# Kernel tuning notes

Measured on AMD Instinct MI355X. Metric: run time of the kernel, lower is better.

## Reference

```python
import jax, jax.numpy as jnp
from jax import lax
import numpy as np

B, L, D, H, SH = 4, 1024, 512, 8, 256
MLP_H = 4 * D
GAMMA, BETA = 0.1, 1.0
SIG_A, SIG_B = 1.0, 0.5
BIG = 1e9


def setup_inputs() -> dict:
    key = jax.random.key(0)
    ks = jax.random.split(key, 8)

    def lin(k, fin, fout):
        return jax.random.normal(k, (fin, fout), jnp.float32) * (1.0 / np.sqrt(fin))

    inp = {}
    inp["x"] = jax.random.normal(ks[0], (B, L, D), jnp.float32)
    inp["ln1_g"] = jnp.ones((D,), jnp.float32)
    inp["ln1_b"] = jnp.zeros((D,), jnp.float32)
    inp["ln2_g"] = jnp.ones((D,), jnp.float32)
    inp["ln2_b"] = jnp.zeros((D,), jnp.float32)
    inp["qkv_w"] = lin(ks[1], D, 3 * D)
    inp["qkv_b"] = jnp.zeros((3 * D,), jnp.float32)
    inp["proj_w"] = lin(ks[2], D, D)
    inp["proj_b"] = jnp.zeros((D,), jnp.float32)
    inp["fc1_w"] = lin(ks[3], D, MLP_H)
    inp["fc1_b"] = jnp.zeros((MLP_H,), jnp.float32)
    inp["fc2_w"] = lin(ks[4], MLP_H, D)
    inp["fc2_b"] = jnp.zeros((D,), jnp.float32)
    # 4 SigmaNets (norm1, attn, norm2, mlp) stacked on leading axis
    inp["sig_w1"] = jax.random.normal(ks[5], (4, D, SH), jnp.float32) * (1.0 / np.sqrt(D))
    inp["sig_b1"] = jnp.zeros((4, SH), jnp.float32)
    inp["sig_w2"] = jax.random.normal(ks[6], (4, SH, D), jnp.float32) * (1.0 / np.sqrt(SH))
    inp["sig_b2"] = jnp.zeros((4, D), jnp.float32)
    return inp


def layernorm(x, g, b, eps=1e-5):
    m = x.mean(-1, keepdims=True)
    v = ((x - m) ** 2).mean(-1, keepdims=True)
    return (x - m) / jnp.sqrt(v + eps) * g + b


def sigmanet(x, w1, b1, w2, b2):
    # (B,L,D) -> (B,L,1), sigma = a*sigmoid(mean(fc2(relu(fc1(x))))) + b
    h = jax.nn.relu(x @ w1 + b1)
    o = h @ w2 + b2
    m = o.mean(-1, keepdims=True)
    return SIG_A * jax.nn.sigmoid(m) + SIG_B


def attention(x, qkv_w, qkv_b, proj_w, proj_b):
    b_, l_, d_ = x.shape
    hd = d_ // H
    qkv = (x @ qkv_w + qkv_b).reshape(b_, l_, 3, H, hd)
    q, k, v = qkv[:, :, 0], qkv[:, :, 1], qkv[:, :, 2]  # (B,L,H,hd)
    scores = jnp.einsum("bqhd,bkhd->bhqk", q, k) * (hd ** -0.5)
    attn = jax.nn.softmax(scores, axis=-1)
    out = jnp.einsum("bhqk,bkhd->bqhd", attn, v).reshape(b_, l_, d_)
    return out @ proj_w + proj_b


def mlp(x, fc1_w, fc1_b, fc2_w, fc2_b):
    return jax.nn.gelu(x @ fc1_w + fc1_b, approximate=False) @ fc2_w + fc2_b


def soft_dtw(C, gamma):
    # soft-min DP over (B, N, N) cost matrix via anti-diagonal scan
    b_, n_, m_ = C.shape
    i_arr = jnp.arange(n_)

    def step(carry, k):
        d2, d1 = carry  # diagonals k-2, k-1; entry i holds R[i, (k-?)-i]
        j = k - i_arr
        valid = (j >= 0) & (j < m_)
        jc = jnp.clip(j, 0, m_ - 1)
        Cd = jnp.where(valid[None, :], C[:, i_arr, jc], BIG)
        pad = jnp.full((b_, 1), BIG, C.dtype)
        a = jnp.concatenate([pad, d2[:, :-1]], axis=1)  # R[i-1, j-1]
        a = a.at[:, 0].set(jnp.where(k == 0, 0.0, a[:, 0]))  # virtual R[-1,-1]=0
        bdiag = jnp.concatenate([pad, d1[:, :-1]], axis=1)  # R[i-1, j]
        c = d1  # R[i, j-1]
        smin = -gamma * jax.nn.logsumexp(-jnp.stack([a, bdiag, c], 0) / gamma, axis=0)
        new = jnp.where(valid[None, :], Cd + smin, BIG)
        return (d1, new), None

    init = (jnp.full((b_, n_), BIG, C.dtype), jnp.full((b_, n_), BIG, C.dtype))
    (_, last), _ = lax.scan(step, init, jnp.arange(n_ + m_ - 1))
    return last[:, n_ - 1]  # R[N-1, M-1]


def udtw(x, y, sx, sy):
    # pairwise squared distances without (B,L,L,D) intermediate
    x2 = jnp.sum(x * x, -1)  # (B,L)
    y2 = jnp.sum(y * y, -1)
    Dm = x2[:, :, None] + y2[:, None, :] - 2.0 * jnp.einsum("bnd,bmd->bnm", x, y)
    Dm = jnp.maximum(Dm, 0.0)
    Sig = sx ** 2 + jnp.swapaxes(sy, 1, 2) ** 2  # (B,L,L) sigma_i^2 + sigma_j^2
    d = soft_dtw(Dm / Sig, GAMMA)               # uncertainty-weighted distance path
    s = soft_dtw(BETA * jnp.log(Sig), GAMMA)    # sigma regularization path
    return d, s


def reference(x, ln1_g, ln1_b, ln2_g, ln2_b, qkv_w, qkv_b, proj_w, proj_b,
              fc1_w, fc1_b, fc2_w, fc2_b, sig_w1, sig_b1, sig_w2, sig_b2):
    orig = x
    attn_out = attention(layernorm(x, ln1_g, ln1_b), qkv_w, qkv_b, proj_w, proj_b)
    sigma_x = sigmanet(orig, sig_w1[0], sig_b1[0], sig_w2[0], sig_b2[0])
    sigma_attn = sigmanet(attn_out, sig_w1[1], sig_b1[1], sig_w2[1], sig_b2[1])
    d_a, s_a = udtw(orig, attn_out, sigma_x, sigma_attn)
    x = x + attn_out * sigma_attn  # merge_mode == 'mul'
    mlp_out = mlp(layernorm(x, ln2_g, ln2_b), fc1_w, fc1_b, fc2_w, fc2_b)
    sigma_x2 = sigmanet(orig, sig_w1[2], sig_b1[2], sig_w2[2], sig_b2[2])
    sigma_mlp = sigmanet(mlp_out, sig_w1[3], sig_b1[3], sig_w2[3], sig_b2[3])
    d_m, s_m = udtw(orig, mlp_out, sigma_x2, sigma_mlp)
    l_ = x.shape[1]
    aux_loss = (d_a.mean() + s_a.mean() + d_m.mean() + s_m.mean()) / (l_ * l_)
    x = x + mlp_out * sigma_mlp
    return x, aux_loss
```

## Files before the change

kernel.cpp:

```cpp
#include <hip/hip_runtime.h>
#include <math.h>

typedef unsigned short ushort;
typedef __attribute__((ext_vector_type(8))) short short8;
typedef __attribute__((ext_vector_type(4))) short short4v;
typedef __attribute__((ext_vector_type(4))) float f32x4;

#define DEVI static __device__ __forceinline__

constexpr int Bq = 4, Lq = 1024, Dq = 512, Hq = 8, SHq = 256;
constexpr int Mrows = Bq * Lq;
constexpr float BIGF = 1e9f;
constexpr int PSTR = 1048576 + 16;

DEVI float bf2f(ushort u) { union { unsigned u; float f; } v; v.u = ((unsigned)u) << 16; return v.f; }
DEVI float bf2f(short s) { return bf2f((ushort)s); }
DEVI ushort f2bf(float f) {
  union { float f; unsigned u; } v; v.f = f;
  unsigned r = v.u + 0x7fffu + ((v.u >> 16) & 1u);
  return (ushort)(r >> 16);
}
DEVI float wave_sum(float x) { for (int o = 1; o < 64; o <<= 1) x += __shfl_xor(x, o, 64); return x; }
DEVI float readin(const void* p, long i, int isf32) {
  return isf32 ? ((const float*)p)[i] : bf2f(((const ushort*)p)[i]);
}

__global__ void detect_kern(const unsigned* __restrict__ g, int* __restrict__ flag) {
  if (threadIdx.x == 0) flag[0] = (g[0] == 0x3F800000u) ? 1 : 0;
}

struct PrepArgs {
  const void *ln1_g, *ln1_b, *ln2_g, *ln2_b, *qkv_b, *proj_b, *fc1_b, *fc2_b, *sig_b1;
  ushort* csmall;
  const void* x_raw; ushort* x_bf;
  const void *qkv_w, *proj_w, *fc1_w, *fc2_w, *sig_w1;
  ushort *wt_qkv, *wt_proj, *wt_fc1, *wt_fc2, *wt_sig1;
  const void *sig_w2;
  const void *sig_b2;
  float *w2bar, *b2bar;
  const int* flag;
};

DEVI void do_transpose(const void* src, ushort* dst, int R, int C, int bx, int by, int bz, int f,
                       ushort (*t)[65]) {
  const int tx = threadIdx.x & 63, tg = threadIdx.x >> 6;
  const long base = (long)bz * R * C;
  const int r0 = by * 64, c0 = bx * 64;
#pragma unroll
  for (int i = 0; i < 16; ++i) {
    int y = tg * 16 + i;
    float v = readin(src, base + (long)(r0 + y) * C + c0 + tx, f);
    t[y][tx] = f2bf(v);
  }
  __syncthreads();
#pragma unroll
  for (int i = 0; i < 16; ++i) {
    int y = tg * 16 + i;
    dst[base + (long)(c0 + y) * R + r0 + tx] = t[tx][y];
  }
}

__global__ __launch_bounds__(256) void prep_kern(PrepArgs a) {
  __shared__ ushort t[64][65];
  const int bid = blockIdx.x, tid = threadIdx.x;
  const int f = *a.flag;
  if (bid < 9) {
    const int off[10] = {0, 512, 1024, 1536, 2048, 3584, 4096, 6144, 6656, 7680};
    const void* ps[9] = {a.ln1_g, a.ln1_b, a.ln2_g, a.ln2_b, a.qkv_b, a.proj_b, a.fc1_b, a.fc2_b, a.sig_b1};
    const void* s = ps[bid];
    const int n = off[bid + 1] - off[bid];
    for (int i = tid; i < n; i += 256)
      a.csmall[off[bid] + i] = f ? f2bf(((const float*)s)[i]) : ((const ushort*)s)[i];
  } else if (bid < 2057) {
    const long c0 = (long)(bid - 9) * 1024;
    for (int i = tid; i < 1024; i += 256)
      a.x_bf[c0 + i] = f ? f2bf(((const float*)a.x_raw)[c0 + i]) : ((const ushort*)a.x_raw)[c0 + i];
  } else if (bid < 2313) {
    const int wid = tid >> 6, lane = tid & 63;
    const int p = (bid - 2057) * 4 + wid;
    const int k = p & 255, s = p >> 8;
    float acc = 0.f;
#pragma unroll
    for (int i = 0; i < 8; ++i) acc += readin(a.sig_w2, ((long)s * SHq + k) * Dq + lane * 8 + i, f);
    acc = wave_sum(acc);
    if (lane == 0) a.w2bar[s * SHq + k] = acc * (1.f / Dq);
  } else if (bid < 2314) {
    const int wid = tid >> 6, lane = tid & 63;
    float acc = 0.f;
#pragma unroll
    for (int i = 0; i < 8; ++i) acc += readin(a.sig_b2, (long)wid * Dq + lane * 8 + i, f);
    acc = wave_sum(acc);
    if (lane == 0) a.b2bar[wid] = acc * (1.f / Dq);
  } else if (bid < 2506) {
    const int lb = bid - 2314;
    do_transpose(a.qkv_w, a.wt_qkv, 512, 1536, lb % 24, lb / 24, 0, f, t);
  } else if (bid < 2570) {
    const int lb = bid - 2506;
    do_transpose(a.proj_w, a.wt_proj, 512, 512, lb % 8, lb / 8, 0, f, t);
  } else if (bid < 2826) {
    const int lb = bid - 2570;
    do_transpose(a.fc1_w, a.wt_fc1, 512, 2048, lb % 32, lb / 32, 0, f, t);
  } else if (bid < 3082) {
    const int lb = bid - 2826;
    do_transpose(a.fc2_w, a.wt_fc2, 2048, 512, lb % 8, lb / 8, 0, f, t);
  } else {
    const int lb = bid - 3082;
    const int z = lb / 32, rem = lb % 32;
    do_transpose(a.sig_w1, a.wt_sig1, 512, 256, rem % 4, rem / 4, z, f, t);
  }
}

__global__ __launch_bounds__(256) void ln_kern(const ushort* __restrict__ x, const ushort* __restrict__ g,
                                               const ushort* __restrict__ b, ushort* __restrict__ out,
                                               float* __restrict__ x2out) {
  const int row = blockIdx.x * 4 + (threadIdx.x >> 6);
  const int lane = threadIdx.x & 63;
  short8 v = *(const short8*)(x + (long)row * Dq + lane * 8);
  float f[8]; float s = 0.f, s2 = 0.f;
#pragma unroll
  for (int i = 0; i < 8; ++i) { f[i] = bf2f(v[i]); s += f[i]; s2 += f[i] * f[i]; }
  s = wave_sum(s); s2 = wave_sum(s2);
  if (lane == 0) x2out[row] = s2;
  float mean = s * (1.f / Dq);
  float var = s2 * (1.f / Dq) - mean * mean;
  float rstd = rsqrtf(var + 1e-5f);
  short8 gv = *(const short8*)(g + lane * 8);
  short8 bv = *(const short8*)(b + lane * 8);
  short8 o;
#pragma unroll
  for (int i = 0; i < 8; ++i) o[i] = (short)f2bf((f[i] - mean) * rstd * bf2f(gv[i]) + bf2f(bv[i]));
  *(short8*)(out + (long)row * Dq + lane * 8) = o;
}

template<int EPI>
__global__ __launch_bounds__(256) void gemm_kern(
    const ushort* __restrict__ A, int lda, long sA,
    const ushort* __restrict__ Bt, int ldb, long sB,
    const ushort* __restrict__ bias,
    void* __restrict__ Cout, int ldc, long sC, int K,
    const float* __restrict__ vx2, const float* __restrict__ vy2,
    const float* __restrict__ vsx, const float* __restrict__ vsy) {
  constexpr int LDT = 40;
  __shared__ alignas(16) short As[128 * LDT];
  __shared__ alignas(16) short Bs[128 * LDT];
  const int tid = threadIdx.x, lane = tid & 63, wid = tid >> 6;
  const int wr = wid >> 1, wc = wid & 1;
  const int m0 = blockIdx.y * 128, n0 = blockIdx.x * 128;
  const int bz = blockIdx.z;
  const ushort* Ab = A + (long)bz * sA;
  const ushort* Bb = Bt + (long)bz * sB;
  const int sr = tid >> 2, sc = (tid & 3) * 8;
  const int lr = lane & 15, lk = (lane >> 4) * 8;
  f32x4 acc[4][4];
#pragma unroll
  for (int i = 0; i < 4; ++i)
#pragma unroll
    for (int j = 0; j < 4; ++j) acc[i][j] = f32x4{0.f, 0.f, 0.f, 0.f};

  for (int k0 = 0; k0 < K; k0 += 32) {
    short8 a0 = *(const short8*)(Ab + (long)(m0 + sr) * lda + k0 + sc);
    short8 a1 = *(const short8*)(Ab + (long)(m0 + sr + 64) * lda + k0 + sc);
    short8 b0 = *(const short8*)(Bb + (long)(n0 + sr) * ldb + k0 + sc);
    short8 b1 = *(const short8*)(Bb + (long)(n0 + sr + 64) * ldb + k0 + sc);
    __syncthreads();
    *(short8*)&As[sr * LDT + sc] = a0;
    *(short8*)&As[(sr + 64) * LDT + sc] = a1;
    *(short8*)&Bs[sr * LDT + sc] = b0;
    *(short8*)&Bs[(sr + 64) * LDT + sc] = b1;
    __syncthreads();
    short8 af[4], bg[4];
#pragma unroll
    for (int m = 0; m < 4; ++m) af[m] = *(const short8*)&As[(wr * 64 + m * 16 + lr) * LDT + lk];
#pragma unroll
    for (int n = 0; n < 4; ++n) bg[n] = *(const short8*)&Bs[(wc * 64 + n * 16 + lr) * LDT + lk];
#pragma unroll
    for (int m = 0; m < 4; ++m)
#pragma unroll
      for (int n = 0; n < 4; ++n)
        acc[m][n] = __builtin_amdgcn_mfma_f32_16x16x32_bf16(af[m], bg[n], acc[m][n], 0, 0, 0);
  }
  const int lq = (lane >> 4) * 4;
#pragma unroll
  for (int n = 0; n < 4; ++n) {
    const int col = n0 + wc * 64 + n * 16 + lr;
    float bia = 0.f, y2v = 0.f, syv = 0.f;
    if (EPI <= 2) { if (bias) bia = bf2f(bias[col]); }
    if (EPI == 3) { y2v = vy2[(long)bz * Lq + col]; float t = vsy[(long)bz * Lq + col]; syv = t * t; }
#pragma unroll
    for (int m = 0; m < 4; ++m) {
      f32x4 v = acc[m][n];
      if (EPI <= 2) {
#pragma unroll
        for (int q = 0; q < 4; ++q) {
          const int row = m0 + wr * 64 + m * 16 + lq + q;
          float c = v[q] + bia;
          if (EPI == 1) c = fmaxf(c, 0.f);
          if (EPI == 2) c = 0.5f * c * (1.f + erff(c * 0.70710678118654752f));
          ((ushort*)Cout)[(long)bz * sC + (long)row * ldc + col] = f2bf(c);
        }
      } else {
        const int row0 = m0 + wr * 64 + m * 16 + lq;
        f32x4 o;
#pragma unroll
        for (int q = 0; q < 4; ++q) {
          float x2v = vx2[(long)bz * Lq + row0 + q];
          float sxv = vsx[(long)bz * Lq + row0 + q];
          float dm = fmaxf(x2v + y2v - 2.f * v[q], 0.f);
          o[q] = dm / (sxv * sxv + syv);
        }
        *(f32x4*)((float*)Cout + (long)bz * sC + (long)col * 1024 + row0) = o;
      }
    }
  }
}

__global__ __launch_bounds__(256) void attn_kern(const ushort* __restrict__ qkv, ushort* __restrict__ octx) {
  const int qt = blockIdx.x, h = blockIdx.y, b = blockIdx.z;
  const int tid = threadIdx.x, lane = tid & 63, wid = tid >> 6;
  const int lr = lane & 15, lkg = lane >> 4;
  __shared__ alignas(16) short Ks[64 * 72];
  __shared__ alignas(16) short Vt[64 * 72];
  __shared__ alignas(16) short Ps[64 * 72];
  const long qrow0 = (long)b * Lq + qt * 64;
  short8 qf[2];
  {
    const ushort* qp = qkv + (qrow0 + wid * 16 + lr) * 1536 + h * 64;
    qf[0] = *(const short8*)(qp + lkg * 8);
    qf[1] = *(const short8*)(qp + 32 + lkg * 8);
  }
  f32x4 accO[4];
#pragma unroll
  for (int n = 0; n < 4; ++n) accO[n] = f32x4{0.f, 0.f, 0.f, 0.f};
  float mrun[4], lrun[4];
#pragma unroll
  for (int q = 0; q < 4; ++q) { mrun[q] = -1e30f; lrun[q] = 0.f; }

  for (int t = 0; t < 16; ++t) {
    __syncthreads();
#pragma unroll
    for (int i = 0; i < 2; ++i) {
      const int row = (tid >> 3) + i * 32;
      const int c8 = (tid & 7) * 8;
      const long gr = ((long)b * Lq + t * 64 + row) * 1536 + h * 64;
      short8 kv = *(const short8*)(qkv + gr + 512 + c8);
      *(short8*)&Ks[row * 72 + c8] = kv;
      short8 vv = *(const short8*)(qkv + gr + 1024 + c8);
#pragma unroll
      for (int j = 0; j < 8; ++j) Vt[(c8 + j) * 72 + row] = vv[j];
    }
    __syncthreads();
    f32x4 sf[4];
#pragma unroll
    for (int n = 0; n < 4; ++n) {
      sf[n] = f32x4{0.f, 0.f, 0.f, 0.f};
#pragma unroll
      for (int ks = 0; ks < 2; ++ks) {
        short8 bk = *(const short8*)&Ks[(n * 16 + lr) * 72 + ks * 32 + lkg * 8];
        sf[n] = __builtin_amdgcn_mfma_f32_16x16x32_bf16(qf[ks], bk, sf[n], 0, 0, 0);
      }
    }
#pragma unroll
    for (int n = 0; n < 4; ++n)
#pragma unroll
      for (int q = 0; q < 4; ++q) sf[n][q] *= 0.125f;
    float scl[4];
#pragma unroll
    for (int q = 0; q < 4; ++q) {
      float mx = fmaxf(fmaxf(sf[0][q], sf[1][q]), fmaxf(sf[2][q], sf[3][q]));
#pragma unroll
      for (int o = 1; o < 16; o <<= 1) mx = fmaxf(mx, __shfl_xor(mx, o, 64));
      float mnew = fmaxf(mrun[q], mx);
      scl[q] = __expf(mrun[q] - mnew);
      mrun[q] = mnew;
      float rs = 0.f;
#pragma unroll
      for (int n = 0; n < 4; ++n) { float pp = __expf(sf[n][q] - mnew); sf[n][q] = pp; rs += pp; }
#pragma unroll
      for (int o = 1; o < 16; o <<= 1) rs += __shfl_xor(rs, o, 64);
      lrun[q] = lrun[q] * scl[q] + rs;
    }
#pragma unroll
    for (int n = 0; n < 4; ++n)
#pragma unroll
      for (int q = 0; q < 4; ++q) accO[n][q] *= scl[q];
#pragma unroll
    for (int n = 0; n < 4; ++n)
#pragma unroll
      for (int q = 0; q < 4; ++q)
        Ps[(wid * 16 + lkg * 4 + q) * 72 + n * 16 + lr] = (short)f2bf(sf[n][q]);
    short8 pa[2];
    pa[0] = *(const short8*)&Ps[(wid * 16 + lr) * 72 + lkg * 8];
    pa[1] = *(const short8*)&Ps[(wid * 16 + lr) * 72 + 32 + lkg * 8];
#pragma unroll
    for (int n = 0; n < 4; ++n)
#pragma unroll
      for (int ks = 0; ks < 2; ++ks) {
        short8 bv = *(const short8*)&Vt[(n * 16 + lr) * 72 + ks * 32 + lkg * 8];
        accO[n] = __builtin_amdgcn_mfma_f32_16x16x32_bf16(pa[ks], bv, accO[n], 0, 0, 0);
      }
  }
#pragma unroll
  for (int n = 0; n < 4; ++n) {
    const int col = h * 64 + n * 16 + lr;
#pragma unroll
    for (int q = 0; q < 4; ++q) {
      const long row = qrow0 + wid * 16 + lkg * 4 + q;
      octx[row * 512 + col] = f2bf(accO[n][q] / fmaxf(lrun[q], 1e-30f));
    }
  }
}

__global__ __launch_bounds__(256) void rownorm2_kern(const ushort* __restrict__ x, float* __restrict__ out) {
  const int row = blockIdx.x * 4 + (threadIdx.x >> 6), lane = threadIdx.x & 63;
  short8 v = *(const short8*)(x + (long)row * Dq + lane * 8);
  float s = 0.f;
#pragma unroll
  for (int i = 0; i < 8; ++i) { float f = bf2f(v[i]); s += f * f; }
  s = wave_sum(s);
  if (lane == 0) out[row] = s;
}

__global__ __launch_bounds__(256) void sigma_reduce_kern(const ushort* __restrict__ h, const float* __restrict__ w2bar,
                                                         const float* __restrict__ b2bar, int set,
                                                         float* __restrict__ sigma) {
  const int row = blockIdx.x * 4 + (threadIdx.x >> 6), lane = threadIdx.x & 63;
  short4v hv = *(const short4v*)(h + (long)row * SHq + lane * 4);
  float s = 0.f;
#pragma unroll
  for (int i = 0; i < 4; ++i) s += bf2f(hv[i]) * w2bar[lane * 4 + i];
  s = wave_sum(s);
  if (lane == 0) {
    float m = s + b2bar[set];
    sigma[(long)set * Mrows + row] = 1.f / (1.f + __expf(-m)) + 0.5f;
  }
}

__global__ __launch_bounds__(256) void fuse1_kern(const ushort* __restrict__ x, const ushort* __restrict__ attn,
                                                  const float* __restrict__ sig, const ushort* __restrict__ g,
                                                  const ushort* __restrict__ bb, void* __restrict__ x1out,
                                                  ushort* __restrict__ xn2, const int* __restrict__ flag) {
  const int row = blockIdx.x * 4 + (threadIdx.x >> 6), lane = threadIdx.x & 63;
  const int isf32 = *flag;
  const float sg = sig[row];
  short8 xv = *(const short8*)(x + (long)row * Dq + lane * 8);
  short8 av = *(const short8*)(attn + (long)row * Dq + lane * 8);
  float f[8]; float s = 0.f, s2 = 0.f;
#pragma unroll
  for (int i = 0; i < 8; ++i) {
    f[i] = bf2f(xv[i]) + bf2f(av[i]) * sg;
    s += f[i]; s2 += f[i] * f[i];
  }
  if (isf32) {
    float* o32 = (float*)x1out + (long)row * Dq + lane * 8;
    *(f32x4*)o32 = f32x4{f[0], f[1], f[2], f[3]};
    *(f32x4*)(o32 + 4) = f32x4{f[4], f[5], f[6], f[7]};
  } else {
    short8 xo;
#pragma unroll
    for (int i = 0; i < 8; ++i) xo[i] = (short)f2bf(f[i]);
    *(short8*)((ushort*)x1out + (long)row * Dq + lane * 8) = xo;
  }
  s = wave_sum(s); s2 = wave_sum(s2);
  float mean = s * (1.f / Dq);
  float var = s2 * (1.f / Dq) - mean * mean;
  float rstd = rsqrtf(var + 1e-5f);
  short8 gv = *(const short8*)(g + lane * 8);
  short8 bv = *(const short8*)(bb + lane * 8);
  short8 o;
#pragma unroll
  for (int i = 0; i < 8; ++i) o[i] = (short)f2bf((f[i] - mean) * rstd * bf2f(gv[i]) + bf2f(bv[i]));
  *(short8*)(xn2 + (long)row * Dq + lane * 8) = o;
}

__global__ __launch_bounds__(256) void fuse2_kern(const ushort* __restrict__ mlp,
                                                  const float* __restrict__ sig, void* __restrict__ out,
                                                  const int* __restrict__ flag) {
  const int row = blockIdx.x * 4 + (threadIdx.x >> 6), lane = threadIdx.x & 63;
  const int isf32 = *flag;
  const float sg = sig[row];
  short8 mv = *(const short8*)(mlp + (long)row * Dq + lane * 8);
  if (isf32) {
    float* o32 = (float*)out + (long)row * Dq + lane * 8;
    f32x4 a = *(const f32x4*)o32;
    f32x4 b = *(const f32x4*)(o32 + 4);
#pragma unroll
    for (int i = 0; i < 4; ++i) a[i] += bf2f(mv[i]) * sg;
#pragma unroll
    for (int i = 0; i < 4; ++i) b[i] += bf2f(mv[4 + i]) * sg;
    *(f32x4*)o32 = a;
    *(f32x4*)(o32 + 4) = b;
  } else {
    ushort* o16 = (ushort*)out + (long)row * Dq + lane * 8;
    short8 xv = *(const short8*)o16;
    short8 o;
#pragma unroll
    for (int i = 0; i < 8; ++i) o[i] = (short)f2bf(bf2f(xv[i]) + bf2f(mv[i]) * sg);
    *(short8*)o16 = o;
  }
}

__global__ __launch_bounds__(128, 1) void dtw_kern(const float* __restrict__ Cta, const float* __restrict__ Ctm,
                                                   const float* __restrict__ sigma, float* __restrict__ res) {
  const int sid = blockIdx.x >> 2, b = blockIdx.x & 3;
  const int tid = threadIdx.x, lane = tid & 63, wid = tid >> 6;
  const bool isS = (sid & 1);
  __shared__ alignas(16) float smemf[18432];
  constexpr float LN2 = 0.69314718055994531f;

  float cur[16];
#pragma unroll
  for (int r = 0; r < 16; ++r) cur[r] = BIGF;
  float A = BIGF;
  float B = BIGF;
  float D = (lane == 0) ? 0.f : BIGF;

  if (!isS) {
    const float* Ct = ((sid == 0) ? Cta : Ctm) + (long)b * PSTR;

#define PRODUCE2(S0)                                                           \
    {                                                                          \
      f32x4 L[4][8];                                                           \
      _Pragma("unroll")                                                        \
      for (int j = 0; j < 4; ++j) {                                            \
        const int ss = (S0) + j;                                               \
        int cA = 2 * ss - 2 * lane;                                            \
        int cB = cA + 1;                                                       \
        cA = cA < 0 ? 0 : (cA > 1023 ? 1023 : cA);                             \
        cB = cB < 0 ? 0 : (cB > 1023 ? 1023 : cB);                             \
        const float* gA = Ct + (long)cA * 1024 + lane * 16;                    \
        const float* gB = Ct + (long)cB * 1024 + lane * 16;                    \
        _Pragma("unroll")                                                      \
        for (int q = 0; q < 4; ++q) { L[j][q] = *(const f32x4*)(gA + q * 4);   \
                                      L[j][4 + q] = *(const f32x4*)(gB + q * 4); } \
      }                                                                        \
      __builtin_amdgcn_sched_barrier(0);                                       \
      _Pragma("unroll")                                                        \
      for (int j = 0; j < 4; ++j) {                                            \
        float* lp = &smemf[(((S0) + j) & 7) * 2304 + lane * 36];               \
        _Pragma("unroll")                                                      \
        for (int q = 0; q < 4; ++q) { *(f32x4*)(lp + q * 4) = L[j][q];         \
                                      *(f32x4*)(lp + 16 + q * 4) = L[j][4 + q]; } \
      }                                                                        \
    }

#define LOADR(RA, RB, S)                                                       \
    {                                                                          \
      const float* lp = &smemf[((S) & 7) * 2304 + lane * 36];                  \
      _Pragma("unroll")                                                        \
      for (int q = 0; q < 4; ++q) { RA[q] = *(const f32x4*)(lp + q * 4);       \
                                    RB[q] = *(const f32x4*)(lp + 16 + q * 4); } \
    }

#define DCHAIN2(S, RA, RB, CHK)                                                \
    {                                                                          \
      const int c1 = 2 * (S) - 2 * lane;                                       \
      const bool v1 = (unsigned)c1 < 1024u;                                    \
      const bool v2 = (unsigned)(c1 + 1) < 1024u;                              \
      float above = A, diag = D;                                               \
      _Pragma("unroll")                                                        \
      for (int i = 0; i < 16; ++i) {                                           \
        float tmp = cur[i];                                                    \
        float v = RA[i >> 2][i & 3] + fminf(fminf(above, tmp), diag);          \
        cur[i] = (CHK) ? (v1 ? v : tmp) : v;                                   \
        diag = tmp; above = v;                                                 \
      }                                                                        \
      float bot1 = cur[15];                                                    \
      above = B; diag = A;                                                     \
      _Pragma("unroll")                                                        \
      for (int i = 0; i < 16; ++i) {                                           \
        float tmp = cur[i];                                                    \
        float v = RB[i >> 2][i & 3] + fminf(fminf(above, tmp), diag);          \
        cur[i] = (CHK) ? (v2 ? v : tmp) : v;                                   \
        diag = tmp; above = v;                                                 \
      }                                                                        \
      float bot2 = cur[15];                                                    \
      D = B;                                                                   \
      float sA = __shfl_up(bot1, 1, 64);                                       \
      float sB = __shfl_up(bot2, 1, 64);                                       \
      A = (lane == 0) ? BIGF : sA;                                             \
      B = (lane == 0) ? BIGF : sB;                                             \
    }

#define DPHASE4(S0, CHK)                                                       \
    {                                                                          \
      f32x4 pa[4], pb[4], qa[4], qb[4];                                        \
      LOADR(pa, pb, (S0) + 0)                                                  \
      LOADR(qa, qb, (S0) + 1)                                                  \
      DCHAIN2((S0) + 0, pa, pb, CHK)                                           \
      LOADR(pa, pb, (S0) + 2)                                                  \
      DCHAIN2((S0) + 1, qa, qb, CHK)                                           \
      LOADR(qa, qb, (S0) + 3)                                                  \
      DCHAIN2((S0) + 2, pa, pb, CHK)                                           \
      DCHAIN2((S0) + 3, qa, qb, CHK)                                           \
    }

    if (wid == 1) PRODUCE2(0)
    __syncthreads();
#pragma clang loop unroll(disable)
    for (int p = 0; p < 16; ++p) {
      if (wid == 1) { PRODUCE2(4 * p + 4) } else { DPHASE4(4 * p, 1) }
      __syncthreads();
    }
#pragma clang loop unroll(disable)
    for (int p = 16; p < 128; ++p) {
      if (wid == 1) { PRODUCE2(4 * p + 4) } else { DPHASE4(4 * p, 0) }
      __syncthreads();
    }
#pragma clang loop unroll(disable)
    for (int p = 128; p < 144; ++p) {
      if (wid == 1) { if (p < 143) PRODUCE2(4 * p + 4) } else { DPHASE4(4 * p, 1) }
      __syncthreads();
    }
#undef PRODUCE2
#undef LOADR
#undef DCHAIN2
#undef DPHASE4
    if (wid == 0 && lane == 63) res[blockIdx.x] = cur[15];
  } else {
    const int sxset = (sid == 1) ? 0 : 2;
    const float* sxv = sigma + (long)sxset * Mrows + b * Lq;
    const float* syv = sigma + (long)(sxset + 1) * Mrows + b * Lq;
    for (int i = tid; i < Lq; i += 128) { float v = syv[i]; smemf[i] = v * v; }
    __syncthreads();
    if (wid == 1) return;
    float sx2[16];
#pragma unroll
    for (int r = 0; r < 16; ++r) { float t = sxv[16 * lane + r]; sx2[r] = t * t; }
    int ia = -2 * lane; ia = ia < 0 ? 0 : ia;
    int ib = 1 - 2 * lane; ib = ib < 0 ? 0 : ib;
    float syA = smemf[ia], syB = smemf[ib];

#define SSTEP2(S, CHK)                                                         \
    {                                                                          \
      int na = 2 * ((S) + 1) - 2 * lane; na = na < 0 ? 0 : (na > 1023 ? 1023 : na); \
      int nb = na + 1; nb = nb > 1023 ? 1023 : nb;                             \
      float syA_n = smemf[na], syB_n = smemf[nb];                              \
      const int c1 = 2 * (S) - 2 * lane;                                       \
      const bool v1 = (unsigned)c1 < 1024u;                                    \
      const bool v2 = (unsigned)(c1 + 1) < 1024u;                              \
      float above = A, diag = D;                                               \
      _Pragma("unroll")                                                        \
      for (int i = 0; i < 16; ++i) {                                           \
        float tmp = cur[i];                                                    \
        float cv = LN2 * __builtin_amdgcn_logf(sx2[i] + syA);                  \
        float v = cv + fminf(fminf(above, tmp), diag);                         \
        cur[i] = (CHK) ? (v1 ? v : tmp) : v;                                   \
        diag = tmp; above = v;                                                 \
      }                                                                        \
      float bot1 = cur[15];                                                    \
      above = B; diag = A;                                                     \
      _Pragma("unroll")                                                        \
      for (int i = 0; i < 16; ++i) {                                           \
        float tmp = cur[i];                                                    \
        float cv = LN2 * __builtin_amdgcn_logf(sx2[i] + syB);                  \
        float v = cv + fminf(fminf(above, tmp), diag);                         \
        cur[i] = (CHK) ? (v2 ? v : tmp) : v;                                   \
        diag = tmp; above = v;                                                 \
      }                                                                        \
      float bot2 = cur[15];                                                    \
      D = B; syA = syA_n; syB = syB_n;                                         \
      float sA = __shfl_up(bot1, 1, 64);                                       \
      float sB = __shfl_up(bot2, 1, 64);                                       \
      A = (lane == 0) ? BIGF : sA;                                             \
      B = (lane == 0) ? BIGF : sB;                                             \
    }

#pragma clang loop unroll(disable)
    for (int s = 0; s < 63; ++s) SSTEP2(s, 1)
#pragma clang loop unroll(disable)
    for (int s = 63; s < 512; ++s) SSTEP2(s, 0)
#pragma clang loop unroll(disable)
    for (int s = 512; s < 576; ++s) SSTEP2(s, 1)
#undef SSTEP2
    if (lane == 63) res[blockIdx.x] = cur[15];
  }
}

__global__ void aux_kern(const float* __restrict__ res, void* __restrict__ out,
                         const int* __restrict__ flag) {
  if (threadIdx.x == 0) {
    float s = 0.f;
    for (int i = 0; i < 16; ++i) s += res[i];
    float v = s * (0.25f / (1024.f * 1024.f));
    if (*flag) ((float*)out)[(size_t)Mrows * 512] = v;
    else       ((ushort*)out)[(size_t)Mrows * 512] = f2bf(v);
  }
}

extern "C" void kernel_launch(void* const* d_in, const int* in_sizes, int n_in,
                              void* d_out, int out_size, void* d_ws, size_t ws_size,
                              hipStream_t stream) {
  const void* x_raw   = d_in[0];
  const void* ln1_g   = d_in[1];
  const void* ln1_b   = d_in[2];
  const void* ln2_g   = d_in[3];
  const void* ln2_b   = d_in[4];
  const void* qkv_w   = d_in[5];
  const void* qkv_b   = d_in[6];
  const void* proj_w  = d_in[7];
  const void* proj_b  = d_in[8];
  const void* fc1_w   = d_in[9];
  const void* fc1_b   = d_in[10];
  const void* fc2_w   = d_in[11];
  const void* fc2_b   = d_in[12];
  const void* sig_w1  = d_in[13];
  const void* sig_b1  = d_in[14];
  const void* sig_w2  = d_in[15];
  const void* sig_b2  = d_in[16];

  char* p = (char*)d_ws;
  auto alloc = [&](size_t n) { char* r = p; p += (n + 255) & ~(size_t)255; return r; };
  const size_t REGION = (size_t)4 * PSTR * 4;
  int*    flag    = (int*)alloc(256);
  ushort* csmall  = (ushort*)alloc(7680 * 2);
  ushort* x_bf    = (ushort*)alloc((size_t)Mrows * 512 * 2);
  ushort* wt_qkv  = (ushort*)alloc((size_t)1536 * 512 * 2);
  ushort* wt_proj = (ushort*)alloc((size_t)512 * 512 * 2);
  ushort* wt_fc1  = (ushort*)alloc((size_t)2048 * 512 * 2);
  ushort* wt_fc2  = (ushort*)alloc((size_t)512 * 2048 * 2);
  ushort* wt_sig1 = (ushort*)alloc((size_t)4 * 256 * 512 * 2);
  float*  w2bar   = (float*)alloc(4 * 256 * 4);
  float*  b2bar   = (float*)alloc(4 * 4);
  ushort* xnorm   = (ushort*)alloc((size_t)Mrows * 512 * 2);
  char* region1 = alloc(REGION);
  ushort* qkvb     = (ushort*)region1;
  ushort* attn_ctx = (ushort*)(region1 + (size_t)Mrows * 1536 * 2);
  float*  Cta      = (float*)region1;
  ushort* abuf   = (ushort*)alloc((size_t)Mrows * 512 * 2);
  ushort* hsig   = (ushort*)alloc((size_t)Mrows * 256 * 2);
  float*  sigma  = (float*)alloc((size_t)4 * Mrows * 4);
  float*  x2n    = (float*)alloc(Mrows * 4);
  float*  y2a    = (float*)alloc(Mrows * 4);
  float*  y2m    = (float*)alloc(Mrows * 4);
  char* region2 = alloc(REGION);
  ushort* h1  = (ushort*)region2;
  float*  Ctm = (float*)region2;
  float*  dres = (float*)alloc(64 * 4);

  const ushort* c_ln1g = csmall + 0;
  const ushort* c_ln1b = csmall + 512;
  const ushort* c_ln2g = csmall + 1024;
  const ushort* c_ln2b = csmall + 1536;
  const ushort* c_qkvb = csmall + 2048;
  const ushort* c_projb = csmall + 3584;
  const ushort* c_fc1b = csmall + 4096;
  const ushort* c_fc2b = csmall + 6144;
  const ushort* c_sigb1 = csmall + 6656;

  detect_kern<<<1, 64, 0, stream>>>((const unsigned*)ln1_g, flag);
  PrepArgs pa;
  pa.ln1_g = ln1_g; pa.ln1_b = ln1_b; pa.ln2_g = ln2_g; pa.ln2_b = ln2_b;
  pa.qkv_b = qkv_b; pa.proj_b = proj_b; pa.fc1_b = fc1_b; pa.fc2_b = fc2_b; pa.sig_b1 = sig_b1;
  pa.csmall = csmall; pa.x_raw = x_raw; pa.x_bf = x_bf;
  pa.qkv_w = qkv_w; pa.proj_w = proj_w; pa.fc1_w = fc1_w; pa.fc2_w = fc2_w; pa.sig_w1 = sig_w1;
  pa.wt_qkv = wt_qkv; pa.wt_proj = wt_proj; pa.wt_fc1 = wt_fc1; pa.wt_fc2 = wt_fc2; pa.wt_sig1 = wt_sig1;
  pa.sig_w2 = sig_w2; pa.sig_b2 = sig_b2; pa.w2bar = w2bar; pa.b2bar = b2bar; pa.flag = flag;
  prep_kern<<<3210, 256, 0, stream>>>(pa);

  ln_kern<<<Mrows / 4, 256, 0, stream>>>(x_bf, c_ln1g, c_ln1b, xnorm, x2n);
  gemm_kern<0><<<dim3(12, 32, 1), 256, 0, stream>>>(xnorm, 512, 0, wt_qkv, 512, 0, c_qkvb,
                                                    qkvb, 1536, 0, 512, nullptr, nullptr, nullptr, nullptr);
  attn_kern<<<dim3(16, 8, 4), 256, 0, stream>>>(qkvb, attn_ctx);
  gemm_kern<0><<<dim3(4, 32, 1), 256, 0, stream>>>(attn_ctx, 512, 0, wt_proj, 512, 0, c_projb,
                                                   abuf, 512, 0, 512, nullptr, nullptr, nullptr, nullptr);
  gemm_kern<1><<<dim3(2, 32, 1), 256, 0, stream>>>(x_bf, 512, 0, wt_sig1, 512, 0, c_sigb1,
                                                   hsig, 256, 0, 512, nullptr, nullptr, nullptr, nullptr);
  sigma_reduce_kern<<<Mrows / 4, 256, 0, stream>>>(hsig, w2bar, b2bar, 0, sigma);
  gemm_kern<1><<<dim3(2, 32, 1), 256, 0, stream>>>(abuf, 512, 0, wt_sig1 + 1 * 256 * 512, 512, 0, c_sigb1 + 256,
                                                   hsig, 256, 0, 512, nullptr, nullptr, nullptr, nullptr);
  sigma_reduce_kern<<<Mrows / 4, 256, 0, stream>>>(hsig, w2bar + 256, b2bar, 1, sigma);
  rownorm2_kern<<<Mrows / 4, 256, 0, stream>>>(abuf, y2a);
  gemm_kern<3><<<dim3(8, 8, 4), 256, 0, stream>>>(x_bf, 512, (long)1024 * 512, abuf, 512, (long)1024 * 512, nullptr,
                                                  Cta, 1024, (long)PSTR, 512, x2n, y2a, sigma, sigma + Mrows);
  fuse1_kern<<<Mrows / 4, 256, 0, stream>>>(x_bf, abuf, sigma + Mrows, c_ln2g, c_ln2b, d_out, xnorm, flag);
  gemm_kern<2><<<dim3(16, 32, 1), 256, 0, stream>>>(xnorm, 512, 0, wt_fc1, 512, 0, c_fc1b,
                                                    h1, 2048, 0, 512, nullptr, nullptr, nullptr, nullptr);
  gemm_kern<0><<<dim3(4, 32, 1), 256, 0, stream>>>(h1, 2048, 0, wt_fc2, 2048, 0, c_fc2b,
                                                   abuf, 512, 0, 2048, nullptr, nullptr, nullptr, nullptr);
  gemm_kern<1><<<dim3(2, 32, 1), 256, 0, stream>>>(x_bf, 512, 0, wt_sig1 + 2 * 256 * 512, 512, 0, c_sigb1 + 512,
                                                   hsig, 256, 0, 512, nullptr, nullptr, nullptr, nullptr);
  sigma_reduce_kern<<<Mrows / 4, 256, 0, stream>>>(hsig, w2bar + 512, b2bar, 2, sigma);
  gemm_kern<1><<<dim3(2, 32, 1), 256, 0, stream>>>(abuf, 512, 0, wt_sig1 + 3 * 256 * 512, 512, 0, c_sigb1 + 768,
                                                   hsig, 256, 0, 512, nullptr, nullptr, nullptr, nullptr);
  sigma_reduce_kern<<<Mrows / 4, 256, 0, stream>>>(hsig, w2bar + 768, b2bar, 3, sigma);
  rownorm2_kern<<<Mrows / 4, 256, 0, stream>>>(abuf, y2m);
  gemm_kern<3><<<dim3(8, 8, 4), 256, 0, stream>>>(x_bf, 512, (long)1024 * 512, abuf, 512, (long)1024 * 512, nullptr,
                                                  Ctm, 1024, (long)PSTR, 512, x2n, y2m,
                                                  sigma + 2 * Mrows, sigma + 3 * Mrows);
  fuse2_kern<<<Mrows / 4, 256, 0, stream>>>(abuf, sigma + 3 * Mrows, d_out, flag);
  dtw_kern<<<16, 128, 0, stream>>>(Cta, Ctm, sigma, dres);
  aux_kern<<<1, 64, 0, stream>>>(dres, d_out, flag);
}
```

Baseline: 511.9 us.

## Fuse sigma-net reduction and row norms into GEMM epilogues via atomics

Computes the SigmaNet second-layer mean dot product and the squared row norms of GEMM outputs directly in GEMM epilogues, accumulating per-row partials with shuffles and atomicAdd. This removes the sigma_reduce and rownorm2 kernels and the hidden activation buffer. The two SigmaNet passes on x are batched into one launch, and the sigmoid is evaluated where sigma is consumed. The accumulation buffers are zeroed in the prep kernel, and float atomics make summation order nondeterministic.

```diff
diff --git a/kernel.cpp b/kernel.cpp
--- a/kernel.cpp
+++ b/kernel.cpp
@@ -24,6 +24,7 @@
 DEVI float readin(const void* p, long i, int isf32) {
   return isf32 ? ((const float*)p)[i] : bf2f(((const ushort*)p)[i]);
 }
+DEVI float sigm05(float x) { return 1.f / (1.f + __expf(-x)) + 0.5f; }
 
 __global__ void detect_kern(const unsigned* __restrict__ g, int* __restrict__ flag) {
   if (threadIdx.x == 0) flag[0] = (g[0] == 0x3F800000u) ? 1 : 0;
@@ -38,6 +39,7 @@
   const void *sig_w2;
   const void *sig_b2;
   float *w2bar, *b2bar;
+  float *zbuf;
   const int* flag;
 };
 
@@ -103,10 +105,13 @@
   } else if (bid < 3082) {
     const int lb = bid - 2826;
     do_transpose(a.fc2_w, a.wt_fc2, 2048, 512, lb % 8, lb / 8, 0, f, t);
-  } else {
+  } else if (bid < 3210) {
     const int lb = bid - 3082;
     const int z = lb / 32, rem = lb % 32;
     do_transpose(a.sig_w1, a.wt_sig1, 512, 256, rem % 4, rem / 4, z, f, t);
+  } else {
+    const int base = (bid - 3210) * 1024;
+    for (int i = tid; i < 1024; i += 256) a.zbuf[base + i] = 0.f;
   }
 }
 
@@ -138,8 +143,11 @@
     const ushort* __restrict__ Bt, int ldb, long sB,
     const ushort* __restrict__ bias,
     void* __restrict__ Cout, int ldc, long sC, int K,
+    float* __restrict__ ysq,
+    const float* __restrict__ w2bar_base, float* __restrict__ sdot, int setBase, int setStep,
     const float* __restrict__ vx2, const float* __restrict__ vy2,
-    const float* __restrict__ vsx, const float* __restrict__ vsy) {
+    const float* __restrict__ dotx, const float* __restrict__ doty,
+    const float* __restrict__ b2bar, int setx, int sety) {
   constexpr int LDT = 40;
   __shared__ alignas(16) short As[128 * LDT];
   __shared__ alignas(16) short Bs[128 * LDT];
@@ -180,23 +188,43 @@
         acc[m][n] = __builtin_amdgcn_mfma_f32_16x16x32_bf16(af[m], bg[n], acc[m][n], 0, 0, 0);
   }
   const int lq = (lane >> 4) * 4;
+  const int set = (EPI == 1) ? (setBase + bz * setStep) : 0;
+  float pd[4][4];
+  if (EPI == 1 || (EPI == 0 && ysq != nullptr)) {
+#pragma unroll
+    for (int m = 0; m < 4; ++m)
+#pragma unroll
+      for (int q = 0; q < 4; ++q) pd[m][q] = 0.f;
+  }
 #pragma unroll
   for (int n = 0; n < 4; ++n) {
     const int col = n0 + wc * 64 + n * 16 + lr;
-    float bia = 0.f, y2v = 0.f, syv = 0.f;
-    if (EPI <= 2) { if (bias) bia = bf2f(bias[col]); }
-    if (EPI == 3) { y2v = vy2[(long)bz * Lq + col]; float t = vsy[(long)bz * Lq + col]; syv = t * t; }
+    float bia = 0.f, y2v = 0.f, syv = 0.f, w2v = 0.f;
+    if (EPI == 0 || EPI == 2) { if (bias) bia = bf2f(bias[col]); }
+    if (EPI == 1) { bia = bf2f(bias[set * 256 + col]); w2v = w2bar_base[set * SHq + col]; }
+    if (EPI == 3) {
+      y2v = vy2[(long)bz * Lq + col];
+      float t = sigm05(doty[(long)bz * Lq + col] + b2bar[sety]);
+      syv = t * t;
+    }
 #pragma unroll
     for (int m = 0; m < 4; ++m) {
       f32x4 v = acc[m][n];
-      if (EPI <= 2) {
+      if (EPI == 0 || EPI == 2) {
 #pragma unroll
         for (int q = 0; q < 4; ++q) {
           const int row = m0 + wr * 64 + m * 16 + lq + q;
           float c = v[q] + bia;
-          if (EPI == 1) c = fmaxf(c, 0.f);
           if (EPI == 2) c = 0.5f * c * (1.f + erff(c * 0.70710678118654752f));
-          ((ushort*)Cout)[(long)bz * sC + (long)row * ldc + col] = f2bf(c);
+          ushort cb = f2bf(c);
+          ((ushort*)Cout)[(long)bz * sC + (long)row * ldc + col] = cb;
+          if (EPI == 0 && ysq != nullptr) { float cr = bf2f(cb); pd[m][q] += cr * cr; }
+        }
+      } else if (EPI == 1) {
+#pragma unroll
+        for (int q = 0; q < 4; ++q) {
+          float c = fmaxf(v[q] + bia, 0.f);
+          pd[m][q] += f2bf(c) == 0 ? 0.f : bf2f(f2bf(c)) * w2v;
         }
       } else {
         const int row0 = m0 + wr * 64 + m * 16 + lq;
@@ -204,13 +232,27 @@
 #pragma unroll
         for (int q = 0; q < 4; ++q) {
           float x2v = vx2[(long)bz * Lq + row0 + q];
-          float sxv = vsx[(long)bz * Lq + row0 + q];
+          float t = sigm05(dotx[(long)bz * Lq + row0 + q] + b2bar[setx]);
           float dm = fmaxf(x2v + y2v - 2.f * v[q], 0.f);
-          o[q] = dm / (sxv * sxv + syv);
+          o[q] = dm / (t * t + syv);
         }
         *(f32x4*)((float*)Cout + (long)bz * sC + (long)col * 1024 + row0) = o;
       }
     }
+  }
+  if (EPI == 1 || (EPI == 0 && ysq != nullptr)) {
+#pragma unroll
+    for (int m = 0; m < 4; ++m)
+#pragma unroll
+      for (int q = 0; q < 4; ++q) {
+#pragma unroll
+        for (int o = 1; o < 16; o <<= 1) pd[m][q] += __shfl_xor(pd[m][q], o, 64);
+        if (lr == 0) {
+          const int row = m0 + wr * 64 + m * 16 + lq + q;
+          if (EPI == 1) atomicAdd(&sdot[(long)set * Mrows + row], pd[m][q]);
+          else          atomicAdd(&ysq[row], pd[m][q]);
+        }
+      }
   }
 }
 
@@ -310,38 +352,14 @@
   }
 }
 
-__global__ __launch_bounds__(256) void rownorm2_kern(const ushort* __restrict__ x, float* __restrict__ out) {
-  const int row = blockIdx.x * 4 + (threadIdx.x >> 6), lane = threadIdx.x & 63;
-  short8 v = *(const short8*)(x + (long)row * Dq + lane * 8);
-  float s = 0.f;
-#pragma unroll
-  for (int i = 0; i < 8; ++i) { float f = bf2f(v[i]); s += f * f; }
-  s = wave_sum(s);
-  if (lane == 0) out[row] = s;
-}
-
-__global__ __launch_bounds__(256) void sigma_reduce_kern(const ushort* __restrict__ h, const float* __restrict__ w2bar,
-                                                         const float* __restrict__ b2bar, int set,
-                                                         float* __restrict__ sigma) {
-  const int row = blockIdx.x * 4 + (threadIdx.x >> 6), lane = threadIdx.x & 63;
-  short4v hv = *(const short4v*)(h + (long)row * SHq + lane * 4);
-  float s = 0.f;
-#pragma unroll
-  for (int i = 0; i < 4; ++i) s += bf2f(hv[i]) * w2bar[lane * 4 + i];
-  s = wave_sum(s);
-  if (lane == 0) {
-    float m = s + b2bar[set];
-    sigma[(long)set * Mrows + row] = 1.f / (1.f + __expf(-m)) + 0.5f;
-  }
-}
-
 __global__ __launch_bounds__(256) void fuse1_kern(const ushort* __restrict__ x, const ushort* __restrict__ attn,
-                                                  const float* __restrict__ sig, const ushort* __restrict__ g,
+                                                  const float* __restrict__ sdot1, const float* __restrict__ b2bar,
+                                                  const ushort* __restrict__ g,
                                                   const ushort* __restrict__ bb, void* __restrict__ x1out,
                                                   ushort* __restrict__ xn2, const int* __restrict__ flag) {
   const int row = blockIdx.x * 4 + (threadIdx.x >> 6), lane = threadIdx.x & 63;
   const int isf32 = *flag;
-  const float sg = sig[row];
+  const float sg = sigm05(sdot1[row] + b2bar[1]);
   short8 xv = *(const short8*)(x + (long)row * Dq + lane * 8);
   short8 av = *(const short8*)(attn + (long)row * Dq + lane * 8);
   float f[8]; float s = 0.f, s2 = 0.f;
@@ -373,11 +391,11 @@
 }
 
 __global__ __launch_bounds__(256) void fuse2_kern(const ushort* __restrict__ mlp,
-                                                  const float* __restrict__ sig, void* __restrict__ out,
-                                                  const int* __restrict__ flag) {
+                                                  const float* __restrict__ sdot3, const float* __restrict__ b2bar,
+                                                  void* __restrict__ out, const int* __restrict__ flag) {
   const int row = blockIdx.x * 4 + (threadIdx.x >> 6), lane = threadIdx.x & 63;
   const int isf32 = *flag;
-  const float sg = sig[row];
+  const float sg = sigm05(sdot3[row] + b2bar[3]);
   short8 mv = *(const short8*)(mlp + (long)row * Dq + lane * 8);
   if (isf32) {
     float* o32 = (float*)out + (long)row * Dq + lane * 8;
@@ -400,7 +418,8 @@
 }
 
 __global__ __launch_bounds__(128, 1) void dtw_kern(const float* __restrict__ Cta, const float* __restrict__ Ctm,
-                                                   const float* __restrict__ sigma, float* __restrict__ res) {
+                                                   const float* __restrict__ sdot, const float* __restrict__ b2bar,
+                                                   float* __restrict__ res) {
   const int sid = blockIdx.x >> 2, b = blockIdx.x & 3;
   const int tid = threadIdx.x, lane = tid & 63, wid = tid >> 6;
   const bool isS = (sid & 1);
@@ -518,14 +537,15 @@
     if (wid == 0 && lane == 63) res[blockIdx.x] = cur[15];
   } else {
     const int sxset = (sid == 1) ? 0 : 2;
-    const float* sxv = sigma + (long)sxset * Mrows + b * Lq;
-    const float* syv = sigma + (long)(sxset + 1) * Mrows + b * Lq;
-    for (int i = tid; i < Lq; i += 128) { float v = syv[i]; smemf[i] = v * v; }
+    const float bx2 = b2bar[sxset], by2 = b2bar[sxset + 1];
+    const float* dx = sdot + (long)sxset * Mrows + b * Lq;
+    const float* dy = sdot + (long)(sxset + 1) * Mrows + b * Lq;
+    for (int i = tid; i < Lq; i += 128) { float v = sigm05(dy[i] + by2); smemf[i] = v * v; }
     __syncthreads();
     if (wid == 1) return;
     float sx2[16];
 #pragma unroll
-    for (int r = 0; r < 16; ++r) { float t = sxv[16 * lane + r]; sx2[r] = t * t; }
+    for (int r = 0; r < 16; ++r) { float t = sigm05(dx[16 * lane + r] + bx2); sx2[r] = t * t; }
     int ia = -2 * lane; ia = ia < 0 ? 0 : ia;
     int ib = 1 - 2 * lane; ib = ib < 0 ? 0 : ib;
     float syA = smemf[ia], syB = smemf[ib];
@@ -627,11 +647,10 @@
   ushort* attn_ctx = (ushort*)(region1 + (size_t)Mrows * 1536 * 2);
   float*  Cta      = (float*)region1;
   ushort* abuf   = (ushort*)alloc((size_t)Mrows * 512 * 2);
-  ushort* hsig   = (ushort*)alloc((size_t)Mrows * 256 * 2);
-  float*  sigma  = (float*)alloc((size_t)4 * Mrows * 4);
-  float*  x2n    = (float*)alloc(Mrows * 4);
+  float*  sdot   = (float*)alloc((size_t)4 * Mrows * 4);
   float*  y2a    = (float*)alloc(Mrows * 4);
   float*  y2m    = (float*)alloc(Mrows * 4);
+  float*  x2n    = (float*)alloc(Mrows * 4);
   char* region2 = alloc(REGION);
   ushort* h1  = (ushort*)region2;
   float*  Ctm = (float*)region2;
@@ -654,40 +673,32 @@
   pa.csmall = csmall; pa.x_raw = x_raw; pa.x_bf = x_bf;
   pa.qkv_w = qkv_w; pa.proj_w = proj_w; pa.fc1_w = fc1_w; pa.fc2_w = fc2_w; pa.sig_w1 = sig_w1;
   pa.wt_qkv = wt_qkv; pa.wt_proj = wt_proj; pa.wt_fc1 = wt_fc1; pa.wt_fc2 = wt_fc2; pa.wt_sig1 = wt_sig1;
-  pa.sig_w2 = sig_w2; pa.sig_b2 = sig_b2; pa.w2bar = w2bar; pa.b2bar = b2bar; pa.flag = flag;
-  prep_kern<<<3210, 256, 0, stream>>>(pa);
+  pa.sig_w2 = sig_w2; pa.sig_b2 = sig_b2; pa.w2bar = w2bar; pa.b2bar = b2bar;
+  pa.zbuf = sdot; pa.flag = flag;
+  prep_kern<<<3234, 256, 0, stream>>>(pa);
 
   ln_kern<<<Mrows / 4, 256, 0, stream>>>(x_bf, c_ln1g, c_ln1b, xnorm, x2n);
   gemm_kern<0><<<dim3(12, 32, 1), 256, 0, stream>>>(xnorm, 512, 0, wt_qkv, 512, 0, c_qkvb,
-                                                    qkvb, 1536, 0, 512, nullptr, nullptr, nullptr, nullptr);
+      qkvb, 1536, 0, 512, nullptr, nullptr, nullptr, 0, 0, nullptr, nullptr, nullptr, nullptr, nullptr, 0, 0);
   attn_kern<<<dim3(16, 8, 4), 256, 0, stream>>>(qkvb, attn_ctx);
   gemm_kern<0><<<dim3(4, 32, 1), 256, 0, stream>>>(attn_ctx, 512, 0, wt_proj, 512, 0, c_projb,
-                                                   abuf, 512, 0, 512, nullptr, nullptr, nullptr, nullptr);
-  gemm_kern<1><<<dim3(2, 32, 1), 256, 0, stream>>>(x_bf, 512, 0, wt_sig1, 512, 0, c_sigb1,
-                                                   hsig, 256, 0, 512, nullptr, nullptr, nullptr, nullptr);
-  sigma_reduce_kern<<<Mrows / 4, 256, 0, stream>>>(hsig, w2bar, b2bar, 0, sigma);
-  gemm_kern<1><<<dim3(2, 32, 1), 256, 0, stream>>>(abuf, 512, 0, wt_sig1 + 1 * 256 * 512, 512, 0, c_sigb1 + 256,
-                                                   hsig, 256, 0, 512, nullptr, nullptr, nullptr, nullptr);
-  sigma_reduce_kern<<<Mrows / 4, 256, 0, stream>>>(hsig, w2bar + 256, b2bar, 1, sigma);
-  rownorm2_kern<<<Mrows / 4, 256, 0, stream>>>(abuf, y2a);
+      abuf, 512, 0, 512, y2a, nullptr, nullptr, 0, 0, nullptr, nullptr, nullptr, nullptr, nullptr, 0, 0);
+  gemm_kern<1><<<dim3(2, 32, 2), 256, 0, stream>>>(x_bf, 512, 0, wt_sig1, 512, (long)2 * 256 * 512, c_sigb1,
+      nullptr, 0, 0, 512, nullptr, w2bar, sdot, 0, 2, nullptr, nullptr, nullptr, nullptr, nullptr, 0, 0);
+  gemm_kern<1><<<dim3(2, 32, 1), 256, 0, stream>>>(abuf, 512, 0, wt_sig1 + 1 * 256 * 512, 512, 0, c_sigb1,
+      nullptr, 0, 0, 512, nullptr, w2bar, sdot, 1, 0, nullptr, nullptr, nullptr, nullptr, nullptr, 0, 0);
   gemm_kern<3><<<dim3(8, 8, 4), 256, 0, stream>>>(x_bf, 512, (long)1024 * 512, abuf, 512, (long)1024 * 512, nullptr,
-                                                  Cta, 1024, (long)PSTR, 512, x2n, y2a, sigma, sigma + Mrows);
-  fuse1_kern<<<Mrows / 4, 256, 0, stream>>>(x_bf, abuf, sigma + Mrows, c_ln2g, c_ln2b, d_out, xnorm, flag);
+      Cta, 1024, (long)PSTR, 512, nullptr, nullptr, nullptr, 0, 0, x2n, y2a, sdot, sdot + Mrows, b2bar, 0, 1);
+  fuse1_kern<<<Mrows / 4, 256, 0, stream>>>(x_bf, abuf, sdot + Mrows, b2bar, c_ln2g, c_ln2b, d_out, xnorm, flag);
   gemm_kern<2><<<dim3(16, 32, 1), 256, 0, stream>>>(xnorm, 512, 0, wt_fc1, 512, 0, c_fc1b,
-                                                    h1, 2048, 0, 512, nullptr, nullptr, nullptr, nullptr);
+      h1, 2048, 0, 512, nullptr, nullptr, nullptr, 0, 0, nullptr, nullptr, nullptr, nullptr, nullptr, 0, 0);
   gemm_kern<0><<<dim3(4, 32, 1), 256, 0, stream>>>(h1, 2048, 0, wt_fc2, 2048, 0, c_fc2b,
-                                                   abuf, 512, 0, 2048, nullptr, nullptr, nullptr, nullptr);
-  gemm_kern<1><<<dim3(2, 32, 1), 256, 0, stream>>>(x_bf, 512, 0, wt_sig1 + 2 * 256 * 512, 512, 0, c_sigb1 + 512,
-                                                   hsig, 256, 0, 512, nullptr, nullptr, nullptr, nullptr);
-  sigma_reduce_kern<<<Mrows / 4, 256, 0, stream>>>(hsig, w2bar + 512, b2bar, 2, sigma);
-  gemm_kern<1><<<dim3(2, 32, 1), 256, 0, stream>>>(abuf, 512, 0, wt_sig1 + 3 * 256 * 512, 512, 0, c_sigb1 + 768,
-                                                   hsig, 256, 0, 512, nullptr, nullptr, nullptr, nullptr);
-  sigma_reduce_kern<<<Mrows / 4, 256, 0, stream>>>(hsig, w2bar + 768, b2bar, 3, sigma);
-  rownorm2_kern<<<Mrows / 4, 256, 0, stream>>>(abuf, y2m);
+      abuf, 512, 0, 2048, y2m, nullptr, nullptr, 0, 0, nullptr, nullptr, nullptr, nullptr, nullptr, 0, 0);
+  gemm_kern<1><<<dim3(2, 32, 1), 256, 0, stream>>>(abuf, 512, 0, wt_sig1 + 3 * 256 * 512, 512, 0, c_sigb1,
+      nullptr, 0, 0, 512, nullptr, w2bar, sdot, 3, 0, nullptr, nullptr, nullptr, nullptr, nullptr, 0, 0);
   gemm_kern<3><<<dim3(8, 8, 4), 256, 0, stream>>>(x_bf, 512, (long)1024 * 512, abuf, 512, (long)1024 * 512, nullptr,
-                                                  Ctm, 1024, (long)PSTR, 512, x2n, y2m,
-                                                  sigma + 2 * Mrows, sigma + 3 * Mrows);
-  fuse2_kern<<<Mrows / 4, 256, 0, stream>>>(abuf, sigma + 3 * Mrows, d_out, flag);
-  dtw_kern<<<16, 128, 0, stream>>>(Cta, Ctm, sigma, dres);
+      Ctm, 1024, (long)PSTR, 512, nullptr, nullptr, nullptr, 0, 0, x2n, y2m, sdot + 2 * Mrows, sdot + 3 * Mrows, b2bar, 2, 3);
+  fuse2_kern<<<Mrows / 4, 256, 0, stream>>>(abuf, sdot + 3 * Mrows, b2bar, d_out, flag);
+  dtw_kern<<<16, 128, 0, stream>>>(Cta, Ctm, sdot, b2bar, dres);
   aux_kern<<<1, 64, 0, stream>>>(dres, d_out, flag);
 }
```

After: 499.2 us. 1.03x faster.
